# Kernel tuning notes

Measured on AMD Instinct MI355X. Metric: run time of the kernel, lower is better.

Reference implementation:

```python
import jax, jax.numpy as jnp
import numpy as np

ALPHA = 0.3
D_K = 64


def setup_inputs() -> dict:
    key = jax.random.key(0)
    kq, kk, kv = jax.random.split(key, 3)
    B, H, S, D = 4, 16, 2048, 64
    Q = jax.random.normal(kq, (B, H, S, D), dtype=jnp.float32)
    K = jax.random.normal(kk, (B, H, S, D), dtype=jnp.float32)
    V = jax.random.normal(kv, (B, H, S, D), dtype=jnp.float32)
    attn_mask = jnp.zeros((B, H, S, S), dtype=bool)
    return {"Q": Q, "K": K, "V": V, "attn_mask": attn_mask}


def reference(Q, K, V, attn_mask):
    # scores: [B,H,S,S] = QK^T / sqrt(d_k)
    scores = jnp.einsum("bhqd,bhkd->bhqk", Q, K) / np.sqrt(D_K).astype(np.float32)
    # adj_tanh(x, a) = (e^{ax}-e^{-ax})/(e^{ax}+e^{-ax}) == tanh(a*x)
    attn = jnp.tanh(ALPHA * scores)
    # NOTE: original torch code calls attn.masked_fill(...) (non in-place) and
    # discards the result, so the mask has NO effect on the output. Replicated
    # faithfully: attn_mask is accepted but unused.
    context = jnp.einsum("bhqk,bhkd->bhqd", attn, V)
    return context
```

## Files before the change

### kernel.cpp

```cpp
#include <hip/hip_runtime.h>


constexpr int S_LEN = 2048;
constexpr int DIM   = 64;
constexpr int QT    = 256;
constexpr int KT    = 64;
constexpr int NKT   = S_LEN / KT;

constexpr float C_EXP2 = 0.10820212528f;

typedef __bf16 bf16_t;
typedef bf16_t bf16x8 __attribute__((ext_vector_type(8)));
typedef float  f32x4  __attribute__((ext_vector_type(4)));

__device__ inline bf16x8 to_bf8(float4 a, float4 b) {
    bf16x8 v;
    v[0] = (bf16_t)a.x; v[1] = (bf16_t)a.y; v[2] = (bf16_t)a.z; v[3] = (bf16_t)a.w;
    v[4] = (bf16_t)b.x; v[5] = (bf16_t)b.y; v[6] = (bf16_t)b.z; v[7] = (bf16_t)b.w;
    return v;
}

__device__ inline float tanh_fast(float s) {
    float t = __builtin_amdgcn_exp2f(s * C_EXP2);
    return 1.0f - 2.0f * __builtin_amdgcn_rcpf(t + 1.0f);
}

__device__ inline unsigned pack2_bf16(float p0, float p1) {
    union { bf16_t h[2]; unsigned u; } pk;
    pk.h[0] = (bf16_t)p0; pk.h[1] = (bf16_t)p1;
    return pk.u;
}

__device__ inline void permlane32_swap(unsigned &a, unsigned &b) {
    asm("v_permlane32_swap_b32 %0, %1" : "+v"(a), "+v"(b));
}
__device__ inline void permlane16_swap(unsigned &a, unsigned &b) {
    asm("v_permlane16_swap_b32 %0, %1" : "+v"(a), "+v"(b));
}

__global__ __launch_bounds__(512, 4) void tanh_attn_kernel(
    const float* __restrict__ Q, const float* __restrict__ K,
    const float* __restrict__ V, float* __restrict__ O)
{
    const int tid  = threadIdx.x;
    const int lane = tid & 63;
    const int wv   = tid >> 6;
    const int lr   = lane & 15;
    const int lg   = lane >> 4;

    const int nwg = gridDim.x;
    const int bid = (blockIdx.x & 7) * (nwg >> 3) + (blockIdx.x >> 3);
    const int qtile = bid & 7;
    const int bh    = bid >> 3;
    const int base  = bh * (S_LEN * DIM);
    const int q0    = qtile * QT;

    __shared__ bf16_t Ql[QT * DIM];
    __shared__ bf16_t Kl[2][KT * DIM];
    __shared__ bf16_t Vt[2][DIM * KT];

    const float* Kb = K + base;
    const float* Vb = V + base;

    const int sr  = tid >> 3;
    const int sc8 = (tid & 7) * 8;
    const int sd  = tid & 63;
    const int skv = (tid >> 6) * 8;

    float4 ka, kb2;
    float  vv[8];
    {
        const float* src = Kb + sr * DIM + sc8;
        ka  = *(const float4*)src;
        kb2 = *(const float4*)(src + 4);
        const float* vsrc = Vb + skv * DIM + sd;
        #pragma unroll
        for (int j = 0; j < 8; ++j) vv[j] = vsrc[j * DIM];
    }

    #pragma unroll
    for (int it = 0; it < 4; ++it) {
        int cid = tid + it * 512;
        int r   = cid >> 3;
        int c8  = (cid & 7) * 8;
        const float* src = Q + base + (q0 + r) * DIM + c8;
        float4 a = *(const float4*)src;
        float4 b = *(const float4*)(src + 4);
        *(bf16x8*)&Ql[r * DIM + (c8 ^ ((r & 7) << 3))] = to_bf8(a, b);
    }
    __syncthreads();

    bf16x8 qa[2][2];
    #pragma unroll
    for (int rt = 0; rt < 2; ++rt)
        #pragma unroll
        for (int ks = 0; ks < 2; ++ks) {
            int r = wv * 32 + rt * 16 + lr;
            int c = ks * 32 + lg * 8;
            qa[rt][ks] = *(const bf16x8*)&Ql[r * DIM + (c ^ ((r & 7) << 3))];
        }

    {
        *(bf16x8*)&Kl[0][sr * DIM + (sc8 ^ ((sr & 7) << 3))] = to_bf8(ka, kb2);
        bf16x8 v;
        #pragma unroll
        for (int j = 0; j < 8; ++j) v[j] = (bf16_t)vv[j];
        *(bf16x8*)&Vt[0][sd * KT + (skv ^ ((sd & 7) << 3))] = v;
    }

    f32x4 oacc[2][4] = {};

    #pragma unroll 2
    for (int kt = 0; kt < NKT; ++kt) {
        const int cur = kt & 1;

        __syncthreads();

        if (kt + 1 < NKT) {
            const int k0n = (kt + 1) * KT;
            const float* src = Kb + (k0n + sr) * DIM + sc8;
            ka  = *(const float4*)src;
            kb2 = *(const float4*)(src + 4);
            const float* vsrc = Vb + (k0n + skv) * DIM + sd;
            #pragma unroll
            for (int j = 0; j < 8; ++j) vv[j] = vsrc[j * DIM];
        }

        const bf16_t* Kc = Kl[cur];
        const bf16_t* Vc = Vt[cur];

        f32x4 sacc[2][4] = {};
        __builtin_amdgcn_s_setprio(1);
        #pragma unroll
        for (int ct = 0; ct < 4; ++ct) {
            int r = ct * 16 + lr;
            bf16x8 kf0 = *(const bf16x8*)&Kc[r * DIM + ((lg * 8)      ^ ((r & 7) << 3))];
            bf16x8 kf1 = *(const bf16x8*)&Kc[r * DIM + ((32 + lg * 8) ^ ((r & 7) << 3))];
            #pragma unroll
            for (int rt = 0; rt < 2; ++rt) {
                sacc[rt][ct] = __builtin_amdgcn_mfma_f32_16x16x32_bf16(kf0, qa[rt][0], sacc[rt][ct], 0, 0, 0);
                sacc[rt][ct] = __builtin_amdgcn_mfma_f32_16x16x32_bf16(kf1, qa[rt][1], sacc[rt][ct], 0, 0, 0);
            }
        }
        __builtin_amdgcn_s_setprio(0);

        bf16x8 pa[2][2];
        #pragma unroll
        for (int rt = 0; rt < 2; ++rt) {
            unsigned dm[4][2];
            #pragma unroll
            for (int ct = 0; ct < 4; ++ct) {
                dm[ct][0] = pack2_bf16(tanh_fast(sacc[rt][ct][0]),
                                       tanh_fast(sacc[rt][ct][1]));
                dm[ct][1] = pack2_bf16(tanh_fast(sacc[rt][ct][2]),
                                       tanh_fast(sacc[rt][ct][3]));
            }
            #pragma unroll
            for (int ks = 0; ks < 2; ++ks) {
                union { unsigned u[4]; bf16x8 v; } pw;
                #pragma unroll
                for (int jj = 0; jj < 2; ++jj) {
                    unsigned A = dm[2 * ks][jj];
                    unsigned B = dm[2 * ks + 1][jj];
                    permlane32_swap(A, B);
                    permlane16_swap(A, B);
                    pw.u[jj]     = A;
                    pw.u[2 + jj] = B;
                }
                pa[rt][ks] = pw.v;
            }
        }

        if (kt + 1 < NKT) {
            const int nxt = cur ^ 1;
            *(bf16x8*)&Kl[nxt][sr * DIM + (sc8 ^ ((sr & 7) << 3))] = to_bf8(ka, kb2);
            bf16x8 v;
            #pragma unroll
            for (int j = 0; j < 8; ++j) v[j] = (bf16_t)vv[j];
            *(bf16x8*)&Vt[nxt][sd * KT + (skv ^ ((sd & 7) << 3))] = v;
        }

        __builtin_amdgcn_s_setprio(1);
        #pragma unroll
        for (int dt = 0; dt < 4; ++dt) {
            int d = dt * 16 + lr;
            bf16x8 vf0 = *(const bf16x8*)&Vc[d * KT + ((lg * 8)      ^ ((d & 7) << 3))];
            bf16x8 vf1 = *(const bf16x8*)&Vc[d * KT + ((32 + lg * 8) ^ ((d & 7) << 3))];
            #pragma unroll
            for (int rt = 0; rt < 2; ++rt) {
                oacc[rt][dt] = __builtin_amdgcn_mfma_f32_16x16x32_bf16(pa[rt][0], vf0, oacc[rt][dt], 0, 0, 0);
                oacc[rt][dt] = __builtin_amdgcn_mfma_f32_16x16x32_bf16(pa[rt][1], vf1, oacc[rt][dt], 0, 0, 0);
            }
        }
        __builtin_amdgcn_s_setprio(0);
    }

    #pragma unroll
    for (int rt = 0; rt < 2; ++rt)
        #pragma unroll
        for (int dt = 0; dt < 4; ++dt)
            #pragma unroll
            for (int j = 0; j < 4; ++j) {
                int q = q0 + wv * 32 + rt * 16 + lg * 4 + j;
                int d = dt * 16 + lr;
                O[base + q * DIM + d] = oacc[rt][dt][j];
            }
}

extern "C" void kernel_launch(void* const* d_in, const int* in_sizes, int n_in,
                              void* d_out, int out_size, void* d_ws, size_t ws_size,
                              hipStream_t stream) {
    const float* Q = (const float*)d_in[0];
    const float* K = (const float*)d_in[1];
    const float* V = (const float*)d_in[2];
    float* O = (float*)d_out;
    dim3 grid(64 * (S_LEN / QT));
    dim3 block(512);
    hipLaunchKernelGGL(tanh_attn_kernel, grid, block, 0, stream, Q, K, V, O);
}
```

Baseline: 113.7 us.

## Skew half the waves by one K-tile to overlap GEMM1 with tanh/GEMM2

Waves 4-7 now run a software-pipelined schedule: each iteration they apply tanh and GEMM2 to the previous tile's scores, then compute GEMM1 for the current tile. Waves 0-3 keep the original order, so at any time the two halves of the block are in different phases. This aims to interleave MFMA work with the VALU-bound tanh across waves. V gets a third LDS buffer so the lagging waves can still read the previous tile, and there is one extra loop iteration. Q is now loaded from global memory straight into registers instead of being staged through LDS, which frees LDS and removes one barrier.

```diff
diff --git a/kernel.cpp b/kernel.cpp
--- a/kernel.cpp
+++ b/kernel.cpp
@@ -13,6 +13,9 @@
 typedef bf16_t bf16x8 __attribute__((ext_vector_type(8)));
 typedef float  f32x4  __attribute__((ext_vector_type(4)));
 
+typedef f32x4 sacc_t[2][4];
+typedef bf16x8 pa_t[2][2];
+
 __device__ inline bf16x8 to_bf8(float4 a, float4 b) {
     bf16x8 v;
     v[0] = (bf16_t)a.x; v[1] = (bf16_t)a.y; v[2] = (bf16_t)a.z; v[3] = (bf16_t)a.w;
@@ -36,6 +39,75 @@
 }
 __device__ inline void permlane16_swap(unsigned &a, unsigned &b) {
     asm("v_permlane16_swap_b32 %0, %1" : "+v"(a), "+v"(b));
+}
+
+__device__ __forceinline__ void gemm1(const bf16_t* __restrict__ Kc,
+                                      const bf16x8 (&qa)[2][2],
+                                      sacc_t& sacc, int lr, int lg) {
+    #pragma unroll
+    for (int rt = 0; rt < 2; ++rt)
+        #pragma unroll
+        for (int ct = 0; ct < 4; ++ct)
+            sacc[rt][ct] = f32x4{0.f, 0.f, 0.f, 0.f};
+    __builtin_amdgcn_s_setprio(1);
+    #pragma unroll
+    for (int ct = 0; ct < 4; ++ct) {
+        int r = ct * 16 + lr;
+        bf16x8 kf0 = *(const bf16x8*)&Kc[r * DIM + ((lg * 8)      ^ ((r & 7) << 3))];
+        bf16x8 kf1 = *(const bf16x8*)&Kc[r * DIM + ((32 + lg * 8) ^ ((r & 7) << 3))];
+        #pragma unroll
+        for (int rt = 0; rt < 2; ++rt) {
+            sacc[rt][ct] = __builtin_amdgcn_mfma_f32_16x16x32_bf16(kf0, qa[rt][0], sacc[rt][ct], 0, 0, 0);
+            sacc[rt][ct] = __builtin_amdgcn_mfma_f32_16x16x32_bf16(kf1, qa[rt][1], sacc[rt][ct], 0, 0, 0);
+        }
+    }
+    __builtin_amdgcn_s_setprio(0);
+}
+
+__device__ __forceinline__ void tanh_redist(const sacc_t& sacc, pa_t& pa) {
+    #pragma unroll
+    for (int rt = 0; rt < 2; ++rt) {
+        unsigned dm[4][2];
+        #pragma unroll
+        for (int ct = 0; ct < 4; ++ct) {
+            dm[ct][0] = pack2_bf16(tanh_fast(sacc[rt][ct][0]),
+                                   tanh_fast(sacc[rt][ct][1]));
+            dm[ct][1] = pack2_bf16(tanh_fast(sacc[rt][ct][2]),
+                                   tanh_fast(sacc[rt][ct][3]));
+        }
+        #pragma unroll
+        for (int ks = 0; ks < 2; ++ks) {
+            union { unsigned u[4]; bf16x8 v; } pw;
+            #pragma unroll
+            for (int jj = 0; jj < 2; ++jj) {
+                unsigned A = dm[2 * ks][jj];
+                unsigned B = dm[2 * ks + 1][jj];
+                permlane32_swap(A, B);
+                permlane16_swap(A, B);
+                pw.u[jj]     = A;
+                pw.u[2 + jj] = B;
+            }
+            pa[rt][ks] = pw.v;
+        }
+    }
+}
+
+__device__ __forceinline__ void gemm2(const bf16_t* __restrict__ Vc,
+                                      const pa_t& pa, f32x4 (&oacc)[2][4],
+                                      int lr, int lg) {
+    __builtin_amdgcn_s_setprio(1);
+    #pragma unroll
+    for (int dt = 0; dt < 4; ++dt) {
+        int d = dt * 16 + lr;
+        bf16x8 vf0 = *(const bf16x8*)&Vc[d * KT + ((lg * 8)      ^ ((d & 7) << 3))];
+        bf16x8 vf1 = *(const bf16x8*)&Vc[d * KT + ((32 + lg * 8) ^ ((d & 7) << 3))];
+        #pragma unroll
+        for (int rt = 0; rt < 2; ++rt) {
+            oacc[rt][dt] = __builtin_amdgcn_mfma_f32_16x16x32_bf16(pa[rt][0], vf0, oacc[rt][dt], 0, 0, 0);
+            oacc[rt][dt] = __builtin_amdgcn_mfma_f32_16x16x32_bf16(pa[rt][1], vf1, oacc[rt][dt], 0, 0, 0);
+        }
+    }
+    __builtin_amdgcn_s_setprio(0);
 }
 
 __global__ __launch_bounds__(512, 4) void tanh_attn_kernel(
@@ -55,9 +127,8 @@
     const int base  = bh * (S_LEN * DIM);
     const int q0    = qtile * QT;
 
-    __shared__ bf16_t Ql[QT * DIM];
     __shared__ bf16_t Kl[2][KT * DIM];
-    __shared__ bf16_t Vt[2][DIM * KT];
+    __shared__ bf16_t Vt[3][DIM * KT];
 
     const float* Kb = K + base;
     const float* Vb = V + base;
@@ -78,26 +149,16 @@
         for (int j = 0; j < 8; ++j) vv[j] = vsrc[j * DIM];
     }
 
-    #pragma unroll
-    for (int it = 0; it < 4; ++it) {
-        int cid = tid + it * 512;
-        int r   = cid >> 3;
-        int c8  = (cid & 7) * 8;
-        const float* src = Q + base + (q0 + r) * DIM + c8;
-        float4 a = *(const float4*)src;
-        float4 b = *(const float4*)(src + 4);
-        *(bf16x8*)&Ql[r * DIM + (c8 ^ ((r & 7) << 3))] = to_bf8(a, b);
-    }
-    __syncthreads();
-
     bf16x8 qa[2][2];
     #pragma unroll
     for (int rt = 0; rt < 2; ++rt)
         #pragma unroll
         for (int ks = 0; ks < 2; ++ks) {
-            int r = wv * 32 + rt * 16 + lr;
-            int c = ks * 32 + lg * 8;
-            qa[rt][ks] = *(const bf16x8*)&Ql[r * DIM + (c ^ ((r & 7) << 3))];
+            const float* src = Q + base + (q0 + wv * 32 + rt * 16 + lr) * DIM
+                               + ks * 32 + lg * 8;
+            float4 a = *(const float4*)src;
+            float4 b = *(const float4*)(src + 4);
+            qa[rt][ks] = to_bf8(a, b);
         }
 
     {
@@ -107,17 +168,20 @@
         for (int j = 0; j < 8; ++j) v[j] = (bf16_t)vv[j];
         *(bf16x8*)&Vt[0][sd * KT + (skv ^ ((sd & 7) << 3))] = v;
     }
+    __syncthreads();
 
     f32x4 oacc[2][4] = {};
-
-    #pragma unroll 2
-    for (int kt = 0; kt < NKT; ++kt) {
-        const int cur = kt & 1;
-
-        __syncthreads();
-
-        if (kt + 1 < NKT) {
-            const int k0n = (kt + 1) * KT;
+    sacc_t sacc;
+    pa_t pa;
+
+    int vCur = 0;
+
+    for (int p = 0; p < NKT + 1; ++p) {
+        const int vPrev = (vCur == 0) ? 2 : vCur - 1;
+        const int vNext = (vCur == 2) ? 0 : vCur + 1;
+
+        if (p + 1 < NKT) {
+            const int k0n = (p + 1) * KT;
             const float* src = Kb + (k0n + sr) * DIM + sc8;
             ka  = *(const float4*)src;
             kb2 = *(const float4*)(src + 4);
@@ -126,73 +190,31 @@
             for (int j = 0; j < 8; ++j) vv[j] = vsrc[j * DIM];
         }
 
-        const bf16_t* Kc = Kl[cur];
-        const bf16_t* Vc = Vt[cur];
-
-        f32x4 sacc[2][4] = {};
-        __builtin_amdgcn_s_setprio(1);
-        #pragma unroll
-        for (int ct = 0; ct < 4; ++ct) {
-            int r = ct * 16 + lr;
-            bf16x8 kf0 = *(const bf16x8*)&Kc[r * DIM + ((lg * 8)      ^ ((r & 7) << 3))];
-            bf16x8 kf1 = *(const bf16x8*)&Kc[r * DIM + ((32 + lg * 8) ^ ((r & 7) << 3))];
-            #pragma unroll
-            for (int rt = 0; rt < 2; ++rt) {
-                sacc[rt][ct] = __builtin_amdgcn_mfma_f32_16x16x32_bf16(kf0, qa[rt][0], sacc[rt][ct], 0, 0, 0);
-                sacc[rt][ct] = __builtin_amdgcn_mfma_f32_16x16x32_bf16(kf1, qa[rt][1], sacc[rt][ct], 0, 0, 0);
-            }
-        }
-        __builtin_amdgcn_s_setprio(0);
-
-        bf16x8 pa[2][2];
-        #pragma unroll
-        for (int rt = 0; rt < 2; ++rt) {
-            unsigned dm[4][2];
-            #pragma unroll
-            for (int ct = 0; ct < 4; ++ct) {
-                dm[ct][0] = pack2_bf16(tanh_fast(sacc[rt][ct][0]),
-                                       tanh_fast(sacc[rt][ct][1]));
-                dm[ct][1] = pack2_bf16(tanh_fast(sacc[rt][ct][2]),
-                                       tanh_fast(sacc[rt][ct][3]));
-            }
-            #pragma unroll
-            for (int ks = 0; ks < 2; ++ks) {
-                union { unsigned u[4]; bf16x8 v; } pw;
-                #pragma unroll
-                for (int jj = 0; jj < 2; ++jj) {
-                    unsigned A = dm[2 * ks][jj];
-                    unsigned B = dm[2 * ks + 1][jj];
-                    permlane32_swap(A, B);
-                    permlane16_swap(A, B);
-                    pw.u[jj]     = A;
-                    pw.u[2 + jj] = B;
-                }
-                pa[rt][ks] = pw.v;
-            }
-        }
-
-        if (kt + 1 < NKT) {
-            const int nxt = cur ^ 1;
-            *(bf16x8*)&Kl[nxt][sr * DIM + (sc8 ^ ((sr & 7) << 3))] = to_bf8(ka, kb2);
+        if (wv < 4) {
+            if (p < NKT) {
+                gemm1(Kl[p & 1], qa, sacc, lr, lg);
+                tanh_redist(sacc, pa);
+                gemm2(Vt[vCur], pa, oacc, lr, lg);
+            }
+        } else {
+            if (p >= 1) {
+                tanh_redist(sacc, pa);
+                gemm2(Vt[vPrev], pa, oacc, lr, lg);
+            }
+            if (p < NKT) {
+                gemm1(Kl[p & 1], qa, sacc, lr, lg);
+            }
+        }
+
+        if (p + 1 < NKT) {
+            *(bf16x8*)&Kl[(p + 1) & 1][sr * DIM + (sc8 ^ ((sr & 7) << 3))] = to_bf8(ka, kb2);
             bf16x8 v;
             #pragma unroll
             for (int j = 0; j < 8; ++j) v[j] = (bf16_t)vv[j];
-            *(bf16x8*)&Vt[nxt][sd * KT + (skv ^ ((sd & 7) << 3))] = v;
-        }
-
-        __builtin_amdgcn_s_setprio(1);
-        #pragma unroll
-        for (int dt = 0; dt < 4; ++dt) {
-            int d = dt * 16 + lr;
-            bf16x8 vf0 = *(const bf16x8*)&Vc[d * KT + ((lg * 8)      ^ ((d & 7) << 3))];
-            bf16x8 vf1 = *(const bf16x8*)&Vc[d * KT + ((32 + lg * 8) ^ ((d & 7) << 3))];
-            #pragma unroll
-            for (int rt = 0; rt < 2; ++rt) {
-                oacc[rt][dt] = __builtin_amdgcn_mfma_f32_16x16x32_bf16(pa[rt][0], vf0, oacc[rt][dt], 0, 0, 0);
-                oacc[rt][dt] = __builtin_amdgcn_mfma_f32_16x16x32_bf16(pa[rt][1], vf1, oacc[rt][dt], 0, 0, 0);
-            }
-        }
-        __builtin_amdgcn_s_setprio(0);
+            *(bf16x8*)&Vt[vNext][sd * KT + (skv ^ ((sd & 7) << 3))] = v;
+        }
+        __syncthreads();
+        vCur = vNext;
     }
 
     #pragma unroll
```

New measurement: 128.1 us. +12.7%, slower.
